# Kernel tuning notes

Hardware: AMD Instinct MI355X
Metric: run time of the kernel (lower is better)

## Reference

```python
import jax, jax.numpy as jnp
import numpy as np

IN_DIM = 8192
OUT_DIM = 8192
BATCH = 2048


def setup_inputs() -> dict:
    key = jax.random.key(0)
    k1, k2, k3, k4 = jax.random.split(key, 4)
    x = jax.random.uniform(k1, (BATCH, IN_DIM), dtype=jnp.float32)  # soft bits in [0,1]
    weights = jax.random.normal(k2, (OUT_DIM, 16), dtype=jnp.float32)
    idx_a = jax.random.randint(k3, (OUT_DIM,), 0, IN_DIM, dtype=jnp.int64)
    idx_b = jax.random.randint(k4, (OUT_DIM,), 0, IN_DIM, dtype=jnp.int64)
    return {"x": x, "weights": weights, "idx_a": idx_a, "idx_b": idx_b}


def _gate_values(a, b):
    # The 16 real-valued relaxations of the 2-input binary logic gates.
    ab = a * b
    return [
        jnp.zeros_like(a),      # 0:  False
        ab,                     # 1:  a AND b
        a - ab,                 # 2:  a AND NOT b
        a,                      # 3:  a
        b - ab,                 # 4:  NOT a AND b
        b,                      # 5:  b
        a + b - 2.0 * ab,       # 6:  a XOR b
        a + b - ab,             # 7:  a OR b
        1.0 - (a + b - ab),     # 8:  NOT (a OR b)
        1.0 - (a + b - 2.0 * ab),  # 9: NOT (a XOR b)
        1.0 - b,                # 10: NOT b
        1.0 - b + ab,           # 11: a OR NOT b
        1.0 - a,                # 12: NOT a
        1.0 - a + ab,           # 13: NOT a OR b
        1.0 - ab,               # 14: NOT (a AND b)
        jnp.ones_like(a),       # 15: True
    ]


def reference(x, weights, idx_a, idx_b):
    # training=True path of LogicLayer.forward_python
    a = x[:, idx_a]  # [B, OUT]
    b = x[:, idx_b]  # [B, OUT]
    w = jax.nn.softmax(weights, axis=-1)  # [OUT, 16]
    gates = _gate_values(a, b)
    out = jnp.zeros_like(a)
    for k in range(16):  # fixed small structural loop over the 16 gates
        out = out + w[None, :, k] * gates[k]
    return out
```

## Files before the change

kernel.cpp:

```cpp
#include <hip/hip_runtime.h>

#define IN_DIM 8192
#define OUT_DIM 8192
#define BATCH 2048

__global__ __launch_bounds__(256) void coeff_kernel(
    const float* __restrict__ w,
    float* __restrict__ c0, float* __restrict__ ca,
    float* __restrict__ cb, float* __restrict__ cab)
{
    int j = blockIdx.x * blockDim.x + threadIdx.x;
    if (j >= OUT_DIM) return;

    const float* wj = w + (size_t)j * 16;
    float wv[16];
    float m = -1e30f;
#pragma unroll
    for (int k = 0; k < 16; ++k) { wv[k] = wj[k]; m = fmaxf(m, wv[k]); }
    float s = 0.f;
#pragma unroll
    for (int k = 0; k < 16; ++k) { wv[k] = __expf(wv[k] - m); s += wv[k]; }
    float inv = 1.0f / s;
#pragma unroll
    for (int k = 0; k < 16; ++k) wv[k] *= inv;

    c0[j]  = wv[8] + wv[9] + wv[10] + wv[11] + wv[12] + wv[13] + wv[14] + wv[15];
    ca[j]  = wv[2] + wv[3] + wv[6] + wv[7] - wv[8] - wv[9] - wv[12] - wv[13];
    cb[j]  = wv[4] + wv[5] + wv[6] + wv[7] - wv[8] - wv[9] - wv[10] - wv[11];
    cab[j] = wv[1] - wv[2] - wv[4] - 2.f * wv[6] - wv[7]
           + wv[8] + 2.f * wv[9] + wv[11] + wv[13] - wv[14];
}

__global__ __launch_bounds__(256) void logic_kernel(
    const float* __restrict__ x,
    const int* __restrict__ idx_a,
    const int* __restrict__ idx_b,
    const float* __restrict__ c0, const float* __restrict__ ca,
    const float* __restrict__ cb, const float* __restrict__ cab,
    float* __restrict__ out)
{
    __shared__ float xrow[IN_DIM];

    const int i = blockIdx.x;
    const float4* xr4 = (const float4*)(x + (size_t)i * IN_DIM);
    float4* xs4 = (float4*)xrow;
#pragma unroll
    for (int k = threadIdx.x; k < IN_DIM / 4; k += 256) {
        xs4[k] = xr4[k];
    }
    __syncthreads();

    const int4*   ia4  = (const int4*)idx_a;
    const int4*   ib4  = (const int4*)idx_b;
    const float4* c04  = (const float4*)c0;
    const float4* ca4  = (const float4*)ca;
    const float4* cb4  = (const float4*)cb;
    const float4* cab4 = (const float4*)cab;
    float4* out4 = (float4*)(out + (size_t)i * OUT_DIM);

    for (int j4 = threadIdx.x; j4 < OUT_DIM / 4; j4 += 256) {
        int4 ia = ia4[j4];
        int4 ib = ib4[j4];
        float4 v0 = c04[j4], va = ca4[j4], vb = cb4[j4], vab = cab4[j4];

        float a0 = xrow[ia.x], b0 = xrow[ib.x];
        float a1 = xrow[ia.y], b1 = xrow[ib.y];
        float a2 = xrow[ia.z], b2 = xrow[ib.z];
        float a3 = xrow[ia.w], b3 = xrow[ib.w];

        float4 o;
        o.x = v0.x + va.x * a0 + vb.x * b0 + vab.x * (a0 * b0);
        o.y = v0.y + va.y * a1 + vb.y * b1 + vab.y * (a1 * b1);
        o.z = v0.z + va.z * a2 + vb.z * b2 + vab.z * (a2 * b2);
        o.w = v0.w + va.w * a3 + vb.w * b3 + vab.w * (a3 * b3);
        out4[j4] = o;
    }
}

extern "C" void kernel_launch(void* const* d_in, const int* in_sizes, int n_in,
                              void* d_out, int out_size, void* d_ws, size_t ws_size,
                              hipStream_t stream)
{
    const float* x       = (const float*)d_in[0];
    const float* weights = (const float*)d_in[1];
    const int*   idx_a   = (const int*)d_in[2];
    const int*   idx_b   = (const int*)d_in[3];
    float* out = (float*)d_out;

    float* wsF = (float*)d_ws;
    float* c0  = wsF;
    float* ca  = wsF + OUT_DIM;
    float* cb  = wsF + 2 * OUT_DIM;
    float* cab = wsF + 3 * OUT_DIM;

    coeff_kernel<<<OUT_DIM / 256, 256, 0, stream>>>(weights, c0, ca, cb, cab);
    logic_kernel<<<BATCH, 256, 0, stream>>>(x, idx_a, idx_b, c0, ca, cb, cab, out);
}
```

Baseline: 131.4 us.

## Prefetch indices and coefficients before barrier, use 512 threads and nontemporal stores

Raises the logic kernel to 512 threads per block and loads all per-thread index and coefficient vectors into registers before the shared-memory barrier. These loads can then overlap with the x-row staging. Output stores become nontemporal so the 64 MB result does not pollute cache. The cost is higher register pressure from 4 iterations of 6 vectors each held in registers, which may lower occupancy.

```diff
diff --git a/kernel.cpp b/kernel.cpp
--- a/kernel.cpp
+++ b/kernel.cpp
@@ -3,6 +3,10 @@
 #define IN_DIM 8192
 #define OUT_DIM 8192
 #define BATCH 2048
+#define TPB 512
+#define JITER (OUT_DIM / 4 / TPB)
+
+typedef float fvec4 __attribute__((ext_vector_type(4)));
 
 __global__ __launch_bounds__(256) void coeff_kernel(
     const float* __restrict__ w,
@@ -31,7 +35,7 @@
            + wv[8] + 2.f * wv[9] + wv[11] + wv[13] - wv[14];
 }
 
-__global__ __launch_bounds__(256) void logic_kernel(
+__global__ __launch_bounds__(TPB) void logic_kernel(
     const float* __restrict__ x,
     const int* __restrict__ idx_a,
     const int* __restrict__ idx_b,
@@ -45,10 +49,10 @@
     const float4* xr4 = (const float4*)(x + (size_t)i * IN_DIM);
     float4* xs4 = (float4*)xrow;
 #pragma unroll
-    for (int k = threadIdx.x; k < IN_DIM / 4; k += 256) {
-        xs4[k] = xr4[k];
+    for (int k = 0; k < IN_DIM / 4 / TPB; ++k) {
+        int idx = k * TPB + threadIdx.x;
+        xs4[idx] = xr4[idx];
     }
-    __syncthreads();
 
     const int4*   ia4  = (const int4*)idx_a;
     const int4*   ib4  = (const int4*)idx_b;
@@ -56,24 +60,38 @@
     const float4* ca4  = (const float4*)ca;
     const float4* cb4  = (const float4*)cb;
     const float4* cab4 = (const float4*)cab;
-    float4* out4 = (float4*)(out + (size_t)i * OUT_DIM);
+    fvec4* out4 = (fvec4*)(out + (size_t)i * OUT_DIM);
 
-    for (int j4 = threadIdx.x; j4 < OUT_DIM / 4; j4 += 256) {
-        int4 ia = ia4[j4];
-        int4 ib = ib4[j4];
-        float4 v0 = c04[j4], va = ca4[j4], vb = cb4[j4], vab = cab4[j4];
+    int4   ia[JITER], ib[JITER];
+    float4 v0[JITER], va[JITER], vb[JITER], vab[JITER];
+#pragma unroll
+    for (int it = 0; it < JITER; ++it) {
+        int j4 = it * TPB + threadIdx.x;
+        ia[it]  = ia4[j4];
+        ib[it]  = ib4[j4];
+        v0[it]  = c04[j4];
+        va[it]  = ca4[j4];
+        vb[it]  = cb4[j4];
+        vab[it] = cab4[j4];
+    }
 
-        float a0 = xrow[ia.x], b0 = xrow[ib.x];
-        float a1 = xrow[ia.y], b1 = xrow[ib.y];
-        float a2 = xrow[ia.z], b2 = xrow[ib.z];
-        float a3 = xrow[ia.w], b3 = xrow[ib.w];
+    __syncthreads();
 
-        float4 o;
-        o.x = v0.x + va.x * a0 + vb.x * b0 + vab.x * (a0 * b0);
-        o.y = v0.y + va.y * a1 + vb.y * b1 + vab.y * (a1 * b1);
-        o.z = v0.z + va.z * a2 + vb.z * b2 + vab.z * (a2 * b2);
-        o.w = v0.w + va.w * a3 + vb.w * b3 + vab.w * (a3 * b3);
-        out4[j4] = o;
+#pragma unroll
+    for (int it = 0; it < JITER; ++it) {
+        int j4 = it * TPB + threadIdx.x;
+
+        float a0 = xrow[ia[it].x], b0 = xrow[ib[it].x];
+        float a1 = xrow[ia[it].y], b1 = xrow[ib[it].y];
+        float a2 = xrow[ia[it].z], b2 = xrow[ib[it].z];
+        float a3 = xrow[ia[it].w], b3 = xrow[ib[it].w];
+
+        fvec4 o;
+        o.x = v0[it].x + va[it].x * a0 + vb[it].x * b0 + vab[it].x * (a0 * b0);
+        o.y = v0[it].y + va[it].y * a1 + vb[it].y * b1 + vab[it].y * (a1 * b1);
+        o.z = v0[it].z + va[it].z * a2 + vb[it].z * b2 + vab[it].z * (a2 * b2);
+        o.w = v0[it].w + va[it].w * a3 + vb[it].w * b3 + vab[it].w * (a3 * b3);
+        __builtin_nontemporal_store(o, &out4[j4]);
     }
 }
 
@@ -94,5 +112,5 @@
     float* cab = wsF + 3 * OUT_DIM;
 
     coeff_kernel<<<OUT_DIM / 256, 256, 0, stream>>>(weights, c0, ca, cb, cab);
-    logic_kernel<<<BATCH, 256, 0, stream>>>(x, idx_a, idx_b, c0, ca, cb, cab, out);
+    logic_kernel<<<BATCH, TPB, 0, stream>>>(x, idx_a, idx_b, c0, ca, cb, cab, out);
 }
```

Measured after the change: 123.8 us. -5.8%, faster.
